# Kernel optimization log

Measured on AMD Instinct MI355X. Metric: run time of the kernel, lower is better.

The kernel has to match this reference:

```python
import jax, jax.numpy as jnp
import numpy as np

N = 50000
E = 1600000
D_IN = 128
HID = 128
EPS = 1e-5
NEG_SLOPE = 0.2


def setup_inputs() -> dict:
    key = jax.random.key(0)
    ks = jax.random.split(key, 16)
    s = 1.0 / np.sqrt(D_IN)
    inp = {
        'x': jax.random.normal(ks[0], (N, D_IN), dtype=jnp.float32),
        'edge_index': jax.random.randint(ks[1], (2, E), 0, N, dtype=jnp.int64),
        # layer 0 params
        'W0': jax.random.normal(ks[2], (D_IN, HID), dtype=jnp.float32) * s,
        'att_src0': jax.random.normal(ks[3], (HID,), dtype=jnp.float32) * s,
        'att_dst0': jax.random.normal(ks[4], (HID,), dtype=jnp.float32) * s,
        'bias0': jnp.zeros((HID,), dtype=jnp.float32),
        'gamma0': jnp.ones((HID,), dtype=jnp.float32),
        'beta0': jnp.zeros((HID,), dtype=jnp.float32),
        # layer 1 params
        'W1': jax.random.normal(ks[5], (HID, HID), dtype=jnp.float32) * s,
        'att_src1': jax.random.normal(ks[6], (HID,), dtype=jnp.float32) * s,
        'att_dst1': jax.random.normal(ks[7], (HID,), dtype=jnp.float32) * s,
        'bias1': jnp.zeros((HID,), dtype=jnp.float32),
        'gamma1': jnp.ones((HID,), dtype=jnp.float32),
        'beta1': jnp.zeros((HID,), dtype=jnp.float32),
    }
    return inp


def _gat_conv(x, W, a_src, a_dst, bias, src, dst, n_nodes):
    h = x @ W                                   # [N, HID]
    alpha_src = h @ a_src                       # [N]
    alpha_dst = h @ a_dst                       # [N]
    e = jax.nn.leaky_relu(alpha_src[src] + alpha_dst[dst], NEG_SLOPE)  # [E']
    # numerically stable softmax over edges grouped by destination node
    m = jax.ops.segment_max(e, dst, num_segments=n_nodes)
    ex = jnp.exp(e - m[dst])
    denom = jax.ops.segment_sum(ex, dst, num_segments=n_nodes)
    alpha = ex / denom[dst]                     # [E']
    out = jax.ops.segment_sum(h[src] * alpha[:, None], dst, num_segments=n_nodes)
    return out + bias


def _batch_norm(x, gamma, beta):
    mean = jnp.mean(x, axis=0)
    var = jnp.mean(jnp.square(x - mean), axis=0)  # biased variance (torch BN normalization)
    return gamma * (x - mean) * jax.lax.rsqrt(var + EPS) + beta


def reference(x, edge_index, W0, att_src0, att_dst0, bias0, gamma0, beta0,
              W1, att_src1, att_dst1, bias1, gamma1, beta1):
    n = x.shape[0]
    loops = jnp.arange(n, dtype=edge_index.dtype)
    src = jnp.concatenate([edge_index[0], loops])
    dst = jnp.concatenate([edge_index[1], loops])

    h = _gat_conv(x, W0, att_src0, att_dst0, bias0, src, dst, n)
    h = _batch_norm(h, gamma0, beta0)
    h = jax.nn.relu(h)
    # dropout: identity in eval mode

    h = _gat_conv(h, W1, att_src1, att_dst1, bias1, src, dst, n)
    h = _batch_norm(h, gamma1, beta1)
    h = jax.nn.relu(h)  # last_activation=True
    return h
```

## Files before the change

kernel.cpp:

```cpp
#include <hip/hip_runtime.h>
#include <math.h>

#define HID 128
#define PAD 96
#define NB 196
#define CAP 10240
#define CHUNK 4096
#define AGG_BLOCKS 2048
#define NEG_SLOPE 0.2f
#define EPS 1e-5f

typedef __attribute__((ext_vector_type(8))) short short8;
typedef __attribute__((ext_vector_type(4))) float floatx4;

static __device__ __forceinline__ unsigned bf16_rne(float x) {
    unsigned u = __float_as_uint(x);
    return (u + 0x7fffu + ((u >> 16) & 1u)) >> 16;
}
static __device__ __forceinline__ float bf16lo_f(unsigned u) { return __uint_as_float(u << 16); }
static __device__ __forceinline__ float bf16hi_f(unsigned u) { return __uint_as_float(u & 0xffff0000u); }

__global__ void wt_build(const float* __restrict__ W, unsigned short* __restrict__ Wt,
                         unsigned short* __restrict__ Hb, int N) {
    int t = threadIdx.x;
    if (t < 64) ((unsigned*)(Hb + (size_t)N * HID))[t] = 0u;
    for (int task = t; task < 2048; task += 256) {
        int c = task & 127, k0 = (task >> 7) * 8;
        unsigned v[8];
#pragma unroll
        for (int j = 0; j < 8; ++j) v[j] = bf16_rne(W[(k0 + j) * HID + c]);
        uint4 st;
        st.x = v[0] | (v[1] << 16);
        st.y = v[2] | (v[3] << 16);
        st.z = v[4] | (v[5] << 16);
        st.w = v[6] | (v[7] << 16);
        *(uint4*)&Wt[c * HID + k0] = st;
    }
}

template <bool BN>
__global__ __launch_bounds__(256) void gemm_mfma(
    const float* __restrict__ X, const unsigned short* __restrict__ Wt,
    const float* __restrict__ a_src, const float* __restrict__ a_dst,
    const float* __restrict__ coef,
    unsigned short* __restrict__ Hb, float* __restrict__ asrc, float* __restrict__ adst,
    int N)
{
    int tid = threadIdx.x;
    int wv = tid >> 6, lane = tid & 63;
    int g = lane >> 4, c = lane & 15;
    int r0w = blockIdx.x * 64 + wv * 16;
    int arow = r0w + c;
    bool avalid = arow < N;
    const float* xr = X + (size_t)(avalid ? arow : 0) * HID;

    floatx4 acc[8];
#pragma unroll
    for (int i = 0; i < 8; ++i) acc[i] = (floatx4)0.f;

#pragma unroll
    for (int kc = 0; kc < 4; ++kc) {
        int k0 = kc * 32 + g * 8;
        float xv[8];
        float4 x0 = *(const float4*)&xr[k0];
        float4 x1 = *(const float4*)&xr[k0 + 4];
        xv[0] = x0.x; xv[1] = x0.y; xv[2] = x0.z; xv[3] = x0.w;
        xv[4] = x1.x; xv[5] = x1.y; xv[6] = x1.z; xv[7] = x1.w;
        if (BN) {
            float4 s0 = *(const float4*)&coef[k0];
            float4 s1 = *(const float4*)&coef[k0 + 4];
            float4 h0 = *(const float4*)&coef[HID + k0];
            float4 h1 = *(const float4*)&coef[HID + k0 + 4];
            xv[0] = fmaxf(fmaf(xv[0], s0.x, h0.x), 0.f);
            xv[1] = fmaxf(fmaf(xv[1], s0.y, h0.y), 0.f);
            xv[2] = fmaxf(fmaf(xv[2], s0.z, h0.z), 0.f);
            xv[3] = fmaxf(fmaf(xv[3], s0.w, h0.w), 0.f);
            xv[4] = fmaxf(fmaf(xv[4], s1.x, h1.x), 0.f);
            xv[5] = fmaxf(fmaf(xv[5], s1.y, h1.y), 0.f);
            xv[6] = fmaxf(fmaf(xv[6], s1.z, h1.z), 0.f);
            xv[7] = fmaxf(fmaf(xv[7], s1.w, h1.w), 0.f);
        }
        short8 af;
#pragma unroll
        for (int j = 0; j < 8; ++j) af[j] = avalid ? (short)bf16_rne(xv[j]) : (short)0;

#pragma unroll
        for (int nt = 0; nt < 8; ++nt) {
            short8 bf = *(const short8*)&Wt[(nt * 16 + c) * HID + k0];
            acc[nt] = __builtin_amdgcn_mfma_f32_16x16x32_bf16(af, bf, acc[nt], 0, 0, 0);
        }
    }

    float as_c[8], ad_c[8];
#pragma unroll
    for (int nt = 0; nt < 8; ++nt) {
        as_c[nt] = a_src[nt * 16 + c];
        ad_c[nt] = a_dst[nt * 16 + c];
    }
#pragma unroll
    for (int reg = 0; reg < 4; ++reg) {
        float s = 0.f, d = 0.f;
#pragma unroll
        for (int nt = 0; nt < 8; ++nt) {
            s = fmaf(acc[nt][reg], as_c[nt], s);
            d = fmaf(acc[nt][reg], ad_c[nt], d);
        }
#pragma unroll
        for (int o = 1; o < 16; o <<= 1) {
            s += __shfl_xor(s, o);
            d += __shfl_xor(d, o);
        }
        int crow = r0w + g * 4 + reg;
        if (c == 0 && crow < N) { asrc[crow] = s; adst[crow] = d; }
    }
#pragma unroll
    for (int reg = 0; reg < 4; ++reg) {
        int crow = r0w + g * 4 + reg;
        if (crow < N) {
#pragma unroll
            for (int nt = 0; nt < 8; ++nt)
                Hb[(size_t)crow * HID + nt * 16 + c] = (unsigned short)bf16_rne(acc[nt][reg]);
        }
    }
}

__global__ __launch_bounds__(256) void scatter_part(
    const int* __restrict__ ei, int* __restrict__ bcur,
    unsigned int* __restrict__ bbuf, int E)
{
    __shared__ int lcnt[NB], gbase[NB];
    int tid = threadIdx.x;
    int i0 = blockIdx.x * CHUNK;
    int i1 = i0 + CHUNK; if (i1 > E) i1 = E;
    if (tid < NB) lcnt[tid] = 0;
    __syncthreads();
    for (int i = i0 + tid; i < i1; i += 256)
        atomicAdd(&lcnt[ei[E + i] >> 8], 1);
    __syncthreads();
    if (tid < NB) {
        gbase[tid] = atomicAdd(&bcur[tid], lcnt[tid]);
        lcnt[tid] = 0;
    }
    __syncthreads();
    for (int i = i0 + tid; i < i1; i += 256) {
        int s = ei[i], d = ei[E + i];
        int b = d >> 8;
        int off = atomicAdd(&lcnt[b], 1);
        int pos = gbase[b] + off;
        if (pos < CAP)
            bbuf[(size_t)b * CAP + pos] = ((unsigned)s << 8) | (unsigned)(d & 255);
    }
}

__global__ __launch_bounds__(256) void ell_build(
    const unsigned int* __restrict__ bbuf, const int* __restrict__ bcur,
    int* __restrict__ cnt, int* __restrict__ ell, float* __restrict__ asrc, int N)
{
    __shared__ int stage[256 * PAD];
    __shared__ int scnt[256];
    int tid = threadIdx.x;
    int b = blockIdx.x;
    int base = b << 8;
    int nodes = N - base; if (nodes > 256) nodes = 256;

    if (b == 0 && tid == 0) asrc[N] = -1e30f;

    int4 s4; s4.x = s4.y = s4.z = s4.w = N;
    for (int idx = tid * 4; idx < 256 * PAD; idx += 1024)
        *(int4*)&stage[idx] = s4;
    __syncthreads();
    for (int i = tid; i < nodes; i += 256) {
        stage[i * PAD] = base + i;
        scnt[i] = 1;
    }
    __syncthreads();

    int nb = bcur[b]; if (nb > CAP) nb = CAP;
    const unsigned int* buf = bbuf + (size_t)b * CAP;
    for (int j = tid; j < nb; j += 256) {
        unsigned int v = buf[j];
        int dl = (int)(v & 255u);
        int s = (int)(v >> 8);
        int p = atomicAdd(&scnt[dl], 1);
        if (p < PAD) stage[dl * PAD + p] = s;
    }
    __syncthreads();

    int total = nodes * PAD;
    int* dst = ell + (size_t)base * PAD;
    for (int idx = tid * 4; idx < total; idx += 1024)
        *(int4*)&dst[idx] = *(const int4*)&stage[idx];
    for (int i = tid; i < nodes; i += 256)
        cnt[base + i] = scnt[i];
}

__global__ __launch_bounds__(256) void gat_aggregate(
    const unsigned short* __restrict__ Hb, const float* __restrict__ asrc,
    const float* __restrict__ adst, const int* __restrict__ cnt,
    const int* __restrict__ ell, const float* __restrict__ bias,
    float* __restrict__ OUT, float* __restrict__ stat, int N)
{
    __shared__ float sbuf[4][HID], qbuf[4][HID];
    int tid = threadIdx.x, wv = tid >> 6, lane = tid & 63;
    int h = lane >> 5, li = lane & 31;
    int c0 = 4 * li;
    float4 b4 = *(const float4*)&bias[c0];
    float ss0 = 0.f, ss1 = 0.f, ss2 = 0.f, ss3 = 0.f;
    float qq0 = 0.f, qq1 = 0.f, qq2 = 0.f, qq3 = 0.f;

    for (int n = blockIdx.x * 4 + wv; n < N; n += AGG_BLOCKS * 4) {
        int nn = __builtin_amdgcn_readfirstlane(n);
        int deg = cnt[nn]; if (deg > PAD) deg = PAD;
        const int* row = ell + (size_t)nn * PAD;
        float adn = adst[nn];
        float a0 = 0.f, a1 = 0.f, a2 = 0.f, a3 = 0.f, den = 0.f;

        for (int j = 0; j < deg; j += 16) {
            int4 s0 = *(const int4*)&row[j];
            int4 s1 = *(const int4*)&row[j + 4];
            int4 s2 = *(const int4*)&row[j + 8];
            int4 s3 = *(const int4*)&row[j + 12];
            int e0 = h ? s0.y : s0.x;
            int e1 = h ? s0.w : s0.z;
            int e2 = h ? s1.y : s1.x;
            int e3 = h ? s1.w : s1.z;
            int e4 = h ? s2.y : s2.x;
            int e5 = h ? s2.w : s2.z;
            int e6 = h ? s3.y : s3.x;
            int e7 = h ? s3.w : s3.z;
#define PAIR(SI) { int si = (SI);                                     \
            float v = asrc[si] + adn;                                 \
            v = fmaxf(v, v * NEG_SLOPE);                              \
            float w = __expf(v);                                      \
            den += w;                                                 \
            uint2 hv = *(const uint2*)(Hb + (size_t)si * HID + c0);   \
            a0 = fmaf(w, bf16lo_f(hv.x), a0);                         \
            a1 = fmaf(w, bf16hi_f(hv.x), a1);                         \
            a2 = fmaf(w, bf16lo_f(hv.y), a2);                         \
            a3 = fmaf(w, bf16hi_f(hv.y), a3); }
            PAIR(e0) PAIR(e1) PAIR(e2) PAIR(e3)
            PAIR(e4) PAIR(e5) PAIR(e6) PAIR(e7)
#undef PAIR
        }

        den += __shfl_xor(den, 32);
        a0 += __shfl_xor(a0, 32);
        a1 += __shfl_xor(a1, 32);
        a2 += __shfl_xor(a2, 32);
        a3 += __shfl_xor(a3, 32);

        float inv = 1.f / den;
        float o0 = fmaf(a0, inv, b4.x);
        float o1 = fmaf(a1, inv, b4.y);
        float o2 = fmaf(a2, inv, b4.z);
        float o3 = fmaf(a3, inv, b4.w);
        ss0 += o0; ss1 += o1; ss2 += o2; ss3 += o3;
        qq0 = fmaf(o0, o0, qq0); qq1 = fmaf(o1, o1, qq1);
        qq2 = fmaf(o2, o2, qq2); qq3 = fmaf(o3, o3, qq3);
        if (h == 0) {
            float4 st;
            st.x = o0; st.y = o1; st.z = o2; st.w = o3;
            *(float4*)&OUT[(size_t)nn * HID + c0] = st;
        }
    }

    if (h == 0) {
        sbuf[wv][c0] = ss0; sbuf[wv][c0 + 1] = ss1;
        sbuf[wv][c0 + 2] = ss2; sbuf[wv][c0 + 3] = ss3;
        qbuf[wv][c0] = qq0; qbuf[wv][c0 + 1] = qq1;
        qbuf[wv][c0 + 2] = qq2; qbuf[wv][c0 + 3] = qq3;
    }
    __syncthreads();
    if (tid < HID) {
        float t = sbuf[0][tid] + sbuf[1][tid] + sbuf[2][tid] + sbuf[3][tid];
        atomicAdd(&stat[tid], t);
    } else {
        int cc = tid - HID;
        float t = qbuf[0][cc] + qbuf[1][cc] + qbuf[2][cc] + qbuf[3][cc];
        atomicAdd(&stat[HID + cc], t);
    }
}

__global__ void bn_coef(const float* __restrict__ stat, const float* __restrict__ gamma,
                        const float* __restrict__ beta, float* __restrict__ coef,
                        float invN)
{
    int c = threadIdx.x;
    float mean = stat[c] * invN;
    float var = stat[HID + c] * invN - mean * mean;
    float s = gamma[c] * rsqrtf(var + EPS);
    coef[c] = s;
    coef[HID + c] = beta[c] - mean * s;
}

__global__ __launch_bounds__(256) void bn_apply(
    float* __restrict__ X, const float* __restrict__ coef, int N)
{
    int tid = threadIdx.x, lane = tid & 63, wv = tid >> 6;
    int c0 = 2 * lane;
    float s0 = coef[c0], s1 = coef[c0 + 1];
    float h0 = coef[HID + c0], h1 = coef[HID + c0 + 1];
    for (int r = blockIdx.x * 4 + wv; r < N; r += gridDim.x * 4) {
        float2 v = *(float2*)&X[(size_t)r * HID + c0];
        float y0 = fmaxf(fmaf(v.x, s0, h0), 0.f);
        float y1 = fmaxf(fmaf(v.y, s1, h1), 0.f);
        *(float2*)&X[(size_t)r * HID + c0] = make_float2(y0, y1);
    }
}

extern "C" void kernel_launch(void* const* d_in, const int* in_sizes, int n_in,
                              void* d_out, int out_size, void* d_ws, size_t ws_size,
                              hipStream_t stream)
{
    const float* x        = (const float*)d_in[0];
    const int*   ei       = (const int*)d_in[1];
    const float* W0       = (const float*)d_in[2];
    const float* att_src0 = (const float*)d_in[3];
    const float* att_dst0 = (const float*)d_in[4];
    const float* bias0    = (const float*)d_in[5];
    const float* gamma0   = (const float*)d_in[6];
    const float* beta0    = (const float*)d_in[7];
    const float* W1       = (const float*)d_in[8];
    const float* att_src1 = (const float*)d_in[9];
    const float* att_dst1 = (const float*)d_in[10];
    const float* bias1    = (const float*)d_in[11];
    const float* gamma1   = (const float*)d_in[12];
    const float* beta1    = (const float*)d_in[13];

    const int N = in_sizes[0] / HID;
    const int E = in_sizes[1] / 2;
    float* out = (float*)d_out;

    char* wsbase = (char*)d_ws;
    size_t off = 0;
    auto alloc = [&](size_t bytes) -> void* {
        void* p = wsbase + off;
        off += (bytes + 255) & ~(size_t)255;
        return p;
    };
    unsigned short* Hb   = (unsigned short*)alloc((size_t)(N + 1) * HID * 2);
    float*          asrc = (float*)alloc((size_t)(N + 1) * 4);
    float*          adst = (float*)alloc((size_t)N * 4);
    int*            cnt  = (int*)  alloc((size_t)N * 4);
    int*            ell  = (int*)  alloc((size_t)N * PAD * 4);
    unsigned int*   bbuf = (unsigned int*)alloc((size_t)NB * CAP * 4);
    int*            bcur = (int*)  alloc(NB * 4);
    float*          stats = (float*)alloc(4 * HID * 4);
    float*          coef0 = (float*)alloc(2 * HID * 4);
    float*          coef1 = (float*)alloc(2 * HID * 4);
    unsigned short* Wt0  = (unsigned short*)alloc(HID * HID * 2);
    unsigned short* Wt1  = (unsigned short*)alloc(HID * HID * 2);
    float* stat0 = stats;
    float* stat1 = stats + 2 * HID;

    const int gemm_blocks  = (N + 63) / 64;
    const int part_blocks  = (E + CHUNK - 1) / CHUNK;
    const int build_blocks = (N + 255) / 256;
    const float invN = 1.0f / (float)N;

    (void)hipMemsetAsync(bcur, 0, NB * 4, stream);
    (void)hipMemsetAsync(stats, 0, 4 * HID * 4, stream);

    wt_build<<<1, 256, 0, stream>>>(W0, Wt0, Hb, N);
    wt_build<<<1, 256, 0, stream>>>(W1, Wt1, Hb, N);
    scatter_part<<<part_blocks, 256, 0, stream>>>(ei, bcur, bbuf, E);
    ell_build<<<build_blocks, 256, 0, stream>>>(bbuf, bcur, cnt, ell, asrc, N);

    gemm_mfma<false><<<gemm_blocks, 256, 0, stream>>>(
        x, Wt0, att_src0, att_dst0, nullptr, Hb, asrc, adst, N);
    gat_aggregate<<<AGG_BLOCKS, 256, 0, stream>>>(
        Hb, asrc, adst, cnt, ell, bias0, out, stat0, N);
    bn_coef<<<1, HID, 0, stream>>>(stat0, gamma0, beta0, coef0, invN);

    gemm_mfma<true><<<gemm_blocks, 256, 0, stream>>>(
        out, Wt1, att_src1, att_dst1, coef0, Hb, asrc, adst, N);
    gat_aggregate<<<AGG_BLOCKS, 256, 0, stream>>>(
        Hb, asrc, adst, cnt, ell, bias1, out, stat1, N);
    bn_coef<<<1, HID, 0, stream>>>(stat1, gamma1, beta1, coef1, invN);
    bn_apply<<<2048, 256, 0, stream>>>(out, coef1, N);
}
```

Before: 289.9 us.

## Merge weight-transpose launches, add half-chunk tail, double aggregate grid

The two single-block weight-conversion kernels become one two-block launch, which removes one kernel launch. The aggregation loop now handles a final partial chunk of up to 8 edges with a half-size body. This avoids gathering padding entries for a full 16-edge step. The aggregate grid size is doubled to 4096 blocks so more nodes are in flight, at the cost of more code paths and block scheduling.

```diff
diff --git a/kernel.cpp b/kernel.cpp
--- a/kernel.cpp
+++ b/kernel.cpp
@@ -6,7 +6,7 @@
 #define NB 196
 #define CAP 10240
 #define CHUNK 4096
-#define AGG_BLOCKS 2048
+#define AGG_BLOCKS 4096
 #define NEG_SLOPE 0.2f
 #define EPS 1e-5f
 
@@ -20,10 +20,13 @@
 static __device__ __forceinline__ float bf16lo_f(unsigned u) { return __uint_as_float(u << 16); }
 static __device__ __forceinline__ float bf16hi_f(unsigned u) { return __uint_as_float(u & 0xffff0000u); }
 
-__global__ void wt_build(const float* __restrict__ W, unsigned short* __restrict__ Wt,
-                         unsigned short* __restrict__ Hb, int N) {
+__global__ void wt_build2(const float* __restrict__ W0, unsigned short* __restrict__ Wt0,
+                          const float* __restrict__ W1, unsigned short* __restrict__ Wt1,
+                          unsigned short* __restrict__ Hb, int N) {
     int t = threadIdx.x;
-    if (t < 64) ((unsigned*)(Hb + (size_t)N * HID))[t] = 0u;
+    const float* W = blockIdx.x ? W1 : W0;
+    unsigned short* Wt = blockIdx.x ? Wt1 : Wt0;
+    if (blockIdx.x == 0 && t < 64) ((unsigned*)(Hb + (size_t)N * HID))[t] = 0u;
     for (int task = t; task < 2048; task += 256) {
         int c = task & 127, k0 = (task >> 7) * 8;
         unsigned v[8];
@@ -215,33 +218,48 @@
         float adn = adst[nn];
         float a0 = 0.f, a1 = 0.f, a2 = 0.f, a3 = 0.f, den = 0.f;
 
-        for (int j = 0; j < deg; j += 16) {
+#define PAIR(SI) { int si = (SI);                                     \
+        float v = asrc[si] + adn;                                     \
+        v = fmaxf(v, v * NEG_SLOPE);                                  \
+        float w = __expf(v);                                          \
+        den += w;                                                     \
+        uint2 hv = *(const uint2*)(Hb + (size_t)si * HID + c0);       \
+        a0 = fmaf(w, bf16lo_f(hv.x), a0);                             \
+        a1 = fmaf(w, bf16hi_f(hv.x), a1);                             \
+        a2 = fmaf(w, bf16lo_f(hv.y), a2);                             \
+        a3 = fmaf(w, bf16hi_f(hv.y), a3); }
+#define BODY16(J) {                                                   \
+        int4 s0 = *(const int4*)&row[(J)];                            \
+        int4 s1 = *(const int4*)&row[(J) + 4];                        \
+        int4 s2 = *(const int4*)&row[(J) + 8];                        \
+        int4 s3 = *(const int4*)&row[(J) + 12];                       \
+        int e0 = h ? s0.y : s0.x;                                     \
+        int e1 = h ? s0.w : s0.z;                                     \
+        int e2 = h ? s1.y : s1.x;                                     \
+        int e3 = h ? s1.w : s1.z;                                     \
+        int e4 = h ? s2.y : s2.x;                                     \
+        int e5 = h ? s2.w : s2.z;                                     \
+        int e6 = h ? s3.y : s3.x;                                     \
+        int e7 = h ? s3.w : s3.z;                                     \
+        PAIR(e0) PAIR(e1) PAIR(e2) PAIR(e3)                           \
+        PAIR(e4) PAIR(e5) PAIR(e6) PAIR(e7) }
+
+        int j = 0;
+        for (; j + 16 <= deg; j += 16) BODY16(j)
+        int rem = deg - j;
+        if (rem > 8) {
+            BODY16(j)
+        } else if (rem > 0) {
             int4 s0 = *(const int4*)&row[j];
             int4 s1 = *(const int4*)&row[j + 4];
-            int4 s2 = *(const int4*)&row[j + 8];
-            int4 s3 = *(const int4*)&row[j + 12];
             int e0 = h ? s0.y : s0.x;
             int e1 = h ? s0.w : s0.z;
             int e2 = h ? s1.y : s1.x;
             int e3 = h ? s1.w : s1.z;
-            int e4 = h ? s2.y : s2.x;
-            int e5 = h ? s2.w : s2.z;
-            int e6 = h ? s3.y : s3.x;
-            int e7 = h ? s3.w : s3.z;
-#define PAIR(SI) { int si = (SI);                                     \
-            float v = asrc[si] + adn;                                 \
-            v = fmaxf(v, v * NEG_SLOPE);                              \
-            float w = __expf(v);                                      \
-            den += w;                                                 \
-            uint2 hv = *(const uint2*)(Hb + (size_t)si * HID + c0);   \
-            a0 = fmaf(w, bf16lo_f(hv.x), a0);                         \
-            a1 = fmaf(w, bf16hi_f(hv.x), a1);                         \
-            a2 = fmaf(w, bf16lo_f(hv.y), a2);                         \
-            a3 = fmaf(w, bf16hi_f(hv.y), a3); }
             PAIR(e0) PAIR(e1) PAIR(e2) PAIR(e3)
-            PAIR(e4) PAIR(e5) PAIR(e6) PAIR(e7)
+        }
+#undef BODY16
 #undef PAIR
-        }
 
         den += __shfl_xor(den, 32);
         a0 += __shfl_xor(a0, 32);
@@ -361,8 +379,7 @@
     (void)hipMemsetAsync(bcur, 0, NB * 4, stream);
     (void)hipMemsetAsync(stats, 0, 4 * HID * 4, stream);
 
-    wt_build<<<1, 256, 0, stream>>>(W0, Wt0, Hb, N);
-    wt_build<<<1, 256, 0, stream>>>(W1, Wt1, Hb, N);
+    wt_build2<<<2, 256, 0, stream>>>(W0, Wt0, W1, Wt1, Hb, N);
     scatter_part<<<part_blocks, 256, 0, stream>>>(ei, bcur, bbuf, E);
     ell_build<<<build_blocks, 256, 0, stream>>>(bbuf, bcur, cnt, ell, asrc, N);
 
```

After: 355.4 us. +22.6%, slower.
